# Kernel optimization log

Measured on AMD Instinct MI355X. Metric: run time of the kernel, lower is better.

Reference implementation:

```python
import jax, jax.numpy as jnp
import numpy as np

B, N, K = 4, 8192, 16
D_POINTS, D_MODEL, INIT_DIM = 64, 64, 3

def _lin(key, din, dout, bias=True):
    k1, k2 = jax.random.split(key)
    s = 1.0 / np.sqrt(din)
    w = jax.random.uniform(k1, (din, dout), minval=-s, maxval=s, dtype=jnp.float32)
    if not bias:
        return w
    b = jax.random.uniform(k2, (dout,), minval=-s, maxval=s, dtype=jnp.float32)
    return w, b

def setup_inputs() -> dict:
    key = jax.random.key(0)
    ks = jax.random.split(key, 12)
    xyz = jax.random.normal(ks[0], (B, N, INIT_DIM), dtype=jnp.float32)
    features = jax.random.normal(ks[1], (B, N, D_POINTS), dtype=jnp.float32)
    knn_idx = jax.random.randint(ks[2], (B, N, K), 0, N)
    fc1_w, fc1_b = _lin(ks[3], D_POINTS, D_MODEL)
    fc2_w, fc2_b = _lin(ks[4], D_MODEL, D_POINTS)
    d1_w, d1_b = _lin(ks[5], INIT_DIM, D_MODEL)
    d2_w, d2_b = _lin(ks[6], D_MODEL, D_MODEL)
    g1_w, g1_b = _lin(ks[7], D_MODEL, D_MODEL)
    g2_w, g2_b = _lin(ks[8], D_MODEL, D_MODEL)
    wq = _lin(ks[9], D_MODEL, D_MODEL, bias=False)
    wk = _lin(ks[10], D_MODEL, D_MODEL, bias=False)
    wv = _lin(ks[11], D_MODEL, D_MODEL, bias=False)
    return dict(xyz=xyz, features=features, knn_idx=knn_idx,
                fc1_w=fc1_w, fc1_b=fc1_b, fc2_w=fc2_w, fc2_b=fc2_b,
                d1_w=d1_w, d1_b=d1_b, d2_w=d2_w, d2_b=d2_b,
                g1_w=g1_w, g1_b=g1_b, g2_w=g2_w, g2_b=g2_b,
                wq=wq, wk=wk, wv=wv)

def _index_points(x, idx):
    # x: (B, N, D), idx: (B, M, K) -> (B, M, K, D)
    return jax.vmap(lambda xb, ib: xb[ib])(x, idx)

def reference(xyz, features, knn_idx,
              fc1_w, fc1_b, fc2_w, fc2_b,
              d1_w, d1_b, d2_w, d2_b,
              g1_w, g1_b, g2_w, g2_b,
              wq, wk, wv):
    idx = knn_idx[:, :, :K]
    knn_xyz = _index_points(xyz, idx)                      # (B,N,K,3)
    pre = features
    x = features @ fc1_w + fc1_b                           # (B,N,d_model)
    q = x @ wq                                             # (B,N,d_model)
    k = _index_points(x @ wk, idx)                         # (B,N,K,d_model)
    v = _index_points(x @ wv, idx)                         # (B,N,K,d_model)
    rel = xyz[:, :, None, :] - knn_xyz                     # (B,N,K,3)
    pos_enc = jax.nn.relu(rel @ d1_w + d1_b) @ d2_w + d2_b # (B,N,K,d_model)
    h = q[:, :, None, :] - k + pos_enc
    attn = jax.nn.relu(h @ g1_w + g1_b) @ g2_w + g2_b      # (B,N,K,d_model)
    attn = jax.nn.softmax(attn / np.sqrt(D_MODEL), axis=-2)
    res = jnp.einsum('bmnf,bmnf->bmf', attn, v + pos_enc)  # (B,N,d_model)
    res = res @ fc2_w + fc2_b + pre                        # (B,N,d_points)
    return res, attn
```

## Files before the change

### kernel.cpp

```cpp
#include <hip/hip_runtime.h>
#include <hip/hip_bf16.h>

#define B_    4
#define N_    8192
#define TOT   (B_*N_)
#define KNN_  16
#define PPW   8
#define PITCH 80

typedef _Float16 half8  __attribute__((ext_vector_type(8)));
typedef float    floatx4 __attribute__((ext_vector_type(4)));

#define MFMA16(A, Bv, C) __builtin_amdgcn_mfma_f32_16x16x32_f16((A), (Bv), (C), 0, 0, 0)

__device__ __forceinline__ void lds_fence(){
  asm volatile("s_waitcnt lgkmcnt(0)" ::: "memory");
}
__device__ __forceinline__ half8 h8_load_f32(const float* __restrict__ p){
  float4 a = *(const float4*)p;
  float4 b = *(const float4*)(p + 4);
  half8 r;
  r[0] = (_Float16)a.x; r[1] = (_Float16)a.y; r[2] = (_Float16)a.z; r[3] = (_Float16)a.w;
  r[4] = (_Float16)b.x; r[5] = (_Float16)b.y; r[6] = (_Float16)b.z; r[7] = (_Float16)b.w;
  return r;
}
__device__ __forceinline__ void store8f(float* __restrict__ p, half8 v){
  float4 a = {(float)v[0], (float)v[1], (float)v[2], (float)v[3]};
  float4 b = {(float)v[4], (float)v[5], (float)v[6], (float)v[7]};
  *(float4*)p = a;
  *(float4*)(p + 4) = b;
}

__device__ void fill_w64(half8* dst, const float* __restrict__ W, int tid){
  for (int i = tid; i < 512; i += 256){
    int lane = i & 63, nt = (i >> 6) & 3, kt = i >> 8;
    int n  = nt*16 + (lane & 15);
    int kb = kt*32 + ((lane >> 4) & 3)*8;
    half8 v;
    #pragma unroll
    for (int j = 0; j < 8; j++) v[j] = (_Float16)W[(kb + j)*64 + n];
    dst[i] = v;
  }
}
__device__ void fill_d1(half8* dst, const float* __restrict__ W, int tid){
  if (tid < 256){
    int lane = tid & 63, nt = tid >> 6;
    int n  = nt*16 + (lane & 15);
    int kb = ((lane >> 4) & 3)*8;
    half8 v;
    #pragma unroll
    for (int j = 0; j < 8; j++){
      int k = kb + j;
      v[j] = (k < 3) ? (_Float16)W[k*64 + n] : (_Float16)0.0f;
    }
    dst[tid] = v;
  }
}

__global__ __launch_bounds__(256, 2) void k1_qkv(
    const float* __restrict__ feat, const float* __restrict__ fc1w, const float* __restrict__ fc1b,
    const float* __restrict__ wqw, const float* __restrict__ wkw, const float* __restrict__ wvw,
    _Float16* __restrict__ qws, _Float16* __restrict__ kws, _Float16* __restrict__ vws)
{
  __shared__ half8 Sfc1[512], Sq[512], Sk[512], Sv[512];
  __shared__ alignas(16) _Float16 xt[4][16*PITCH];
  const int tid = threadIdx.x;
  fill_w64(Sfc1, fc1w, tid);
  fill_w64(Sq, wqw, tid);
  fill_w64(Sk, wkw, tid);
  fill_w64(Sv, wvw, tid);
  __syncthreads();

  const int wave = tid >> 6, lane = tid & 63, quad = lane >> 4, m16 = lane & 15;
  _Float16* tx = &xt[wave][0];
  const int rowbase = blockIdx.x*64 + wave*16;
  float fb[4];
  #pragma unroll
  for (int nt = 0; nt < 4; nt++) fb[nt] = fc1b[nt*16 + m16];

  const int arow = rowbase + m16;
  half8 Fa0 = h8_load_f32(&feat[arow*64 + quad*8]);
  half8 Fa1 = h8_load_f32(&feat[arow*64 + 32 + quad*8]);
  const floatx4 z4 = {0.f, 0.f, 0.f, 0.f};

  #pragma unroll
  for (int nt = 0; nt < 4; nt++){
    floatx4 acc = MFMA16(Fa0, Sfc1[nt*64 + lane], z4);
    acc = MFMA16(Fa1, Sfc1[(4 + nt)*64 + lane], acc);
    const int col = nt*16 + m16;
    #pragma unroll
    for (int r = 0; r < 4; r++)
      tx[(quad*4 + r)*PITCH + col] = (_Float16)(acc[r] + fb[nt]);
  }
  lds_fence();
  const half8 Ax0 = *(const half8*)&tx[m16*PITCH + quad*8];
  const half8 Ax1 = *(const half8*)&tx[m16*PITCH + 32 + quad*8];

#define EMIT_QKV(S, OUT)                                                      \
  { _Pragma("unroll")                                                         \
    for (int nt = 0; nt < 4; nt++){                                           \
      floatx4 acc = MFMA16(Ax0, S[nt*64 + lane], z4);                         \
      acc = MFMA16(Ax1, S[(4 + nt)*64 + lane], acc);                          \
      _Pragma("unroll")                                                       \
      for (int r = 0; r < 4; r++)                                             \
        OUT[(rowbase + quad*4 + r)*64 + nt*16 + m16] = (_Float16)acc[r];      \
    } }
  EMIT_QKV(Sq, qws)
  EMIT_QKV(Sk, kws)
  EMIT_QKV(Sv, vws)
#undef EMIT_QKV
}

__global__ __launch_bounds__(256, 2) void k2_point(
    const float* __restrict__ xyz, const int* __restrict__ knn,
    const float* __restrict__ d1w, const float* __restrict__ d1b,
    const float* __restrict__ d2w, const float* __restrict__ d2b,
    const float* __restrict__ g1w, const float* __restrict__ g1b,
    const float* __restrict__ g2w, const float* __restrict__ g2b,
    const _Float16* __restrict__ qws, const _Float16* __restrict__ kws,
    const _Float16* __restrict__ vws,
    _Float16* __restrict__ r0, float* __restrict__ attn_out)
{
  __shared__ half8 Sd1[256], Sd2[512], Sg1[512], Sg2[512];
  __shared__ alignas(16) _Float16 tiles[4][2][16*PITCH];
  const int tid = threadIdx.x;
  fill_d1(Sd1, d1w, tid);
  fill_w64(Sd2, d2w, tid);
  fill_w64(Sg1, g1w, tid);
  fill_w64(Sg2, g2w, tid);
  __syncthreads();

  const int wave = tid >> 6, lane = tid & 63, quad = lane >> 4, m16 = lane & 15;
  _Float16* tA = &tiles[wave][0][0];
  _Float16* tB = &tiles[wave][1][0];

  half8 Fd1[4], Fd2[2][4], Fg1[2][4], Fg2[2][4];
  #pragma unroll
  for (int nt = 0; nt < 4; nt++){
    Fd1[nt] = Sd1[nt*64 + lane];
    #pragma unroll
    for (int kt = 0; kt < 2; kt++){
      Fd2[kt][nt] = Sd2[(kt*4 + nt)*64 + lane];
      Fg1[kt][nt] = Sg1[(kt*4 + nt)*64 + lane];
      Fg2[kt][nt] = Sg2[(kt*4 + nt)*64 + lane];
    }
  }
  float bd1[4], bd2[4], bg1[4], bg2[4];
  #pragma unroll
  for (int nt = 0; nt < 4; nt++){
    const int c = nt*16 + m16;
    bd1[nt] = d1b[c]; bd2[nt] = d2b[c];
    bg1[nt] = g1b[c]; bg2[nt] = g2b[c];
  }
  const floatx4 z4 = {0.f, 0.f, 0.f, 0.f};

  for (int p = 0; p < PPW; p++){
    const int gpt  = blockIdx.x*(4*PPW) + wave*PPW + p;
    const int b    = gpt >> 13;
    const int idxm = knn[gpt*KNN_ + m16];
    const int grow = b*N_ + idxm;

    half8 Ar;
    #pragma unroll
    for (int j = 0; j < 8; j++) Ar[j] = (_Float16)0.0f;
    if (quad == 0){
      #pragma unroll
      for (int j = 0; j < 3; j++)
        Ar[j] = (_Float16)(xyz[gpt*3 + j] - xyz[grow*3 + j]);
    }

    #pragma unroll
    for (int nt = 0; nt < 4; nt++){
      floatx4 acc = MFMA16(Ar, Fd1[nt], z4);
      const int col = nt*16 + m16;
      #pragma unroll
      for (int r = 0; r < 4; r++){
        float t = acc[r] + bd1[nt];
        tA[(quad*4 + r)*PITCH + col] = (_Float16)(t > 0.f ? t : 0.f);
      }
    }
    lds_fence();
    const half8 At0 = *(const half8*)&tA[m16*PITCH + quad*8];
    const half8 At1 = *(const half8*)&tA[m16*PITCH + 32 + quad*8];

    #pragma unroll
    for (int nt = 0; nt < 4; nt++){
      floatx4 acc = MFMA16(At0, Fd2[0][nt], z4);
      acc = MFMA16(At1, Fd2[1][nt], acc);
      const int col = nt*16 + m16;
      #pragma unroll
      for (int r = 0; r < 4; r++)
        tB[(quad*4 + r)*PITCH + col] = (_Float16)(acc[r] + bd2[nt]);
    }
    lds_fence();
    const half8 Pa0 = *(const half8*)&tB[m16*PITCH + quad*8];
    const half8 Pa1 = *(const half8*)&tB[m16*PITCH + 32 + quad*8];

    const half8 Ka0 = *(const half8*)&kws[grow*64 + quad*8];
    const half8 Ka1 = *(const half8*)&kws[grow*64 + 32 + quad*8];
    const half8 Qa0 = *(const half8*)&qws[gpt*64 + quad*8];
    const half8 Qa1 = *(const half8*)&qws[gpt*64 + 32 + quad*8];
    const half8 H0 = Qa0 - Ka0 + Pa0;
    const half8 H1 = Qa1 - Ka1 + Pa1;

    #pragma unroll
    for (int nt = 0; nt < 4; nt++){
      floatx4 acc = MFMA16(H0, Fg1[0][nt], z4);
      acc = MFMA16(H1, Fg1[1][nt], acc);
      const int col = nt*16 + m16;
      #pragma unroll
      for (int r = 0; r < 4; r++){
        float t = acc[r] + bg1[nt];
        tA[(quad*4 + r)*PITCH + col] = (_Float16)(t > 0.f ? t : 0.f);
      }
    }
    lds_fence();
    const half8 U0 = *(const half8*)&tA[m16*PITCH + quad*8];
    const half8 U1 = *(const half8*)&tA[m16*PITCH + 32 + quad*8];

    float A2[4][4];
    #pragma unroll
    for (int nt = 0; nt < 4; nt++){
      floatx4 acc = MFMA16(U0, Fg2[0][nt], z4);
      acc = MFMA16(U1, Fg2[1][nt], acc);
      #pragma unroll
      for (int r = 0; r < 4; r++) A2[nt][r] = acc[r] + bg2[nt];
    }

    #pragma unroll
    for (int nt = 0; nt < 4; nt++){
      float mx = fmaxf(fmaxf(A2[nt][0], A2[nt][1]), fmaxf(A2[nt][2], A2[nt][3]));
      mx = fmaxf(mx, __shfl_xor(mx, 16));
      mx = fmaxf(mx, __shfl_xor(mx, 32));
      float s = 0.f;
      #pragma unroll
      for (int r = 0; r < 4; r++){
        float e = expf((A2[nt][r] - mx)*0.125f);
        A2[nt][r] = e; s += e;
      }
      s += __shfl_xor(s, 16);
      s += __shfl_xor(s, 32);
      const float inv = 1.0f / s;
      const int col = nt*16 + m16;
      #pragma unroll
      for (int r = 0; r < 4; r++)
        tA[(quad*4 + r)*PITCH + col] = (_Float16)(A2[nt][r]*inv);
    }
    lds_fence();
    const half8 Aa0 = *(const half8*)&tA[m16*PITCH + quad*8];
    const half8 Aa1 = *(const half8*)&tA[m16*PITCH + 32 + quad*8];
    const half8 Va0 = *(const half8*)&vws[grow*64 + quad*8];
    const half8 Va1 = *(const half8*)&vws[grow*64 + 32 + quad*8];

    float* ap = attn_out + ((size_t)gpt*KNN_ + m16)*64;
    store8f(ap + quad*8, Aa0);
    store8f(ap + 32 + quad*8, Aa1);

    float w0[8], w1[8];
    #pragma unroll
    for (int j = 0; j < 8; j++){
      w0[j] = (float)Aa0[j] * ((float)Va0[j] + (float)Pa0[j]);
      w1[j] = (float)Aa1[j] * ((float)Va1[j] + (float)Pa1[j]);
    }
    #pragma unroll
    for (int mask = 1; mask < 16; mask <<= 1){
      #pragma unroll
      for (int j = 0; j < 8; j++){
        w0[j] += __shfl_xor(w0[j], mask);
        w1[j] += __shfl_xor(w1[j], mask);
      }
    }
    if (m16 == 0){
      half8 o0, o1;
      #pragma unroll
      for (int j = 0; j < 8; j++){ o0[j] = (_Float16)w0[j]; o1[j] = (_Float16)w1[j]; }
      *(half8*)&r0[gpt*64 + quad*8] = o0;
      *(half8*)&r0[gpt*64 + 32 + quad*8] = o1;
    }
  }
}

__global__ __launch_bounds__(256, 2) void k3_fc2(
    const _Float16* __restrict__ r0, const float* __restrict__ fc2w,
    const float* __restrict__ fc2b, const float* __restrict__ feat,
    float* __restrict__ out_res)
{
  __shared__ half8 S[512];
  const int tid = threadIdx.x;
  fill_w64(S, fc2w, tid);
  __syncthreads();

  const int wave = tid >> 6, lane = tid & 63, quad = lane >> 4, m16 = lane & 15;
  const int rowbase = blockIdx.x*64 + wave*16;
  float fb[4];
  #pragma unroll
  for (int nt = 0; nt < 4; nt++) fb[nt] = fc2b[nt*16 + m16];

  const half8 A0 = *(const half8*)&r0[(rowbase + m16)*64 + quad*8];
  const half8 A1 = *(const half8*)&r0[(rowbase + m16)*64 + 32 + quad*8];
  const floatx4 z4 = {0.f, 0.f, 0.f, 0.f};

  #pragma unroll
  for (int nt = 0; nt < 4; nt++){
    floatx4 acc = MFMA16(A0, S[nt*64 + lane], z4);
    acc = MFMA16(A1, S[(4 + nt)*64 + lane], acc);
    #pragma unroll
    for (int r = 0; r < 4; r++){
      const int rowg = rowbase + quad*4 + r;
      const int col  = nt*16 + m16;
      out_res[rowg*64 + col] = acc[r] + fb[nt] + feat[rowg*64 + col];
    }
  }
}

extern "C" void kernel_launch(void* const* d_in, const int* in_sizes, int n_in,
                              void* d_out, int out_size, void* d_ws, size_t ws_size,
                              hipStream_t stream)
{
  (void)in_sizes; (void)n_in; (void)out_size; (void)ws_size;
  const float* xyz  = (const float*)d_in[0];
  const float* feat = (const float*)d_in[1];
  const int*   knn  = (const int*)d_in[2];
  const float* fc1w = (const float*)d_in[3];
  const float* fc1b = (const float*)d_in[4];
  const float* fc2w = (const float*)d_in[5];
  const float* fc2b = (const float*)d_in[6];
  const float* d1w  = (const float*)d_in[7];
  const float* d1b  = (const float*)d_in[8];
  const float* d2w  = (const float*)d_in[9];
  const float* d2b  = (const float*)d_in[10];
  const float* g1w  = (const float*)d_in[11];
  const float* g1b  = (const float*)d_in[12];
  const float* g2w  = (const float*)d_in[13];
  const float* g2b  = (const float*)d_in[14];
  const float* wq   = (const float*)d_in[15];
  const float* wk   = (const float*)d_in[16];
  const float* wv   = (const float*)d_in[17];

  _Float16* ws  = (_Float16*)d_ws;
  _Float16* qws = ws;
  _Float16* kws = ws + (size_t)TOT*64;
  _Float16* vws = ws + (size_t)2*TOT*64;
  _Float16* r0  = ws + (size_t)3*TOT*64;

  float* out      = (float*)d_out;
  float* out_res  = out;
  float* out_attn = out + (size_t)TOT*64;

  k1_qkv<<<TOT/64, 256, 0, stream>>>(feat, fc1w, fc1b, wq, wk, wv, qws, kws, vws);
  k2_point<<<TOT/(4*PPW), 256, 0, stream>>>(xyz, knn, d1w, d1b, d2w, d2b,
                                            g1w, g1b, g2w, g2b,
                                            qws, kws, vws, r0, out_attn);
  k3_fc2<<<TOT/64, 256, 0, stream>>>(r0, fc2w, fc2b, feat, out_res);
}
```

Measured before the change: 268.5 us.

## Load weights directly into registers, shrink LDS tiles, prefetch gathers, use fp16 reduction

k2 and k3 now load their MFMA weight fragments straight from global memory into registers, dropping the LDS weight staging and block barrier. k2 reuses a single tile per wave with a smaller pitch and raises the occupancy hint. It also preloads the kNN indices and issues the K/V/Q gathers at the start of each point iteration to hide latency. The softmax uses exp2 with a folded scale, and the weighted sum over neighbours is reduced with packed half2 shuffles instead of fp32. The fp16 accumulation lowers precision, and register pressure may rise.

```diff
diff --git a/kernel.cpp b/kernel.cpp
--- a/kernel.cpp
+++ b/kernel.cpp
@@ -6,9 +6,11 @@
 #define TOT   (B_*N_)
 #define KNN_  16
 #define PPW   8
-#define PITCH 80
+#define PITCH 68
 
 typedef _Float16 half8  __attribute__((ext_vector_type(8)));
+typedef _Float16 half4  __attribute__((ext_vector_type(4)));
+typedef _Float16 half2v __attribute__((ext_vector_type(2)));
 typedef float    floatx4 __attribute__((ext_vector_type(4)));
 
 #define MFMA16(A, Bv, C) __builtin_amdgcn_mfma_f32_16x16x32_f16((A), (Bv), (C), 0, 0, 0)
@@ -30,6 +32,35 @@
   *(float4*)p = a;
   *(float4*)(p + 4) = b;
 }
+__device__ __forceinline__ half8 tile_read8(const _Float16* t, int idx){
+  half4 lo = *(const half4*)(t + idx);
+  half4 hi = *(const half4*)(t + idx + 4);
+  half8 r;
+  #pragma unroll
+  for (int j = 0; j < 4; j++){ r[j] = lo[j]; r[4+j] = hi[j]; }
+  return r;
+}
+__device__ __forceinline__ half8 wfrag(const float* __restrict__ W, int kb, int n){
+  half8 v;
+  #pragma unroll
+  for (int j = 0; j < 8; j++) v[j] = (_Float16)W[(kb + j)*64 + n];
+  return v;
+}
+__device__ __forceinline__ half8 red_over_m16(half8 x){
+  union { half8 h; int i[4]; } u; u.h = x;
+  #pragma unroll
+  for (int mask = 1; mask < 16; mask <<= 1){
+    #pragma unroll
+    for (int t = 0; t < 4; t++){
+      int o = __shfl_xor(u.i[t], mask);
+      union { int i; half2v h; } a, b;
+      a.i = u.i[t]; b.i = o;
+      a.h = a.h + b.h;
+      u.i[t] = a.i;
+    }
+  }
+  return u.h;
+}
 
 __device__ void fill_w64(half8* dst, const float* __restrict__ W, int tid){
   for (int i = tid; i < 512; i += 256){
@@ -40,20 +71,6 @@
     #pragma unroll
     for (int j = 0; j < 8; j++) v[j] = (_Float16)W[(kb + j)*64 + n];
     dst[i] = v;
-  }
-}
-__device__ void fill_d1(half8* dst, const float* __restrict__ W, int tid){
-  if (tid < 256){
-    int lane = tid & 63, nt = tid >> 6;
-    int n  = nt*16 + (lane & 15);
-    int kb = ((lane >> 4) & 3)*8;
-    half8 v;
-    #pragma unroll
-    for (int j = 0; j < 8; j++){
-      int k = kb + j;
-      v[j] = (k < 3) ? (_Float16)W[k*64 + n] : (_Float16)0.0f;
-    }
-    dst[tid] = v;
   }
 }
 
@@ -93,8 +110,8 @@
       tx[(quad*4 + r)*PITCH + col] = (_Float16)(acc[r] + fb[nt]);
   }
   lds_fence();
-  const half8 Ax0 = *(const half8*)&tx[m16*PITCH + quad*8];
-  const half8 Ax1 = *(const half8*)&tx[m16*PITCH + 32 + quad*8];
+  const half8 Ax0 = tile_read8(tx, m16*PITCH + quad*8);
+  const half8 Ax1 = tile_read8(tx, m16*PITCH + 32 + quad*8);
 
 #define EMIT_QKV(S, OUT)                                                      \
   { _Pragma("unroll")                                                         \
@@ -111,7 +128,7 @@
 #undef EMIT_QKV
 }
 
-__global__ __launch_bounds__(256, 2) void k2_point(
+__global__ __launch_bounds__(256, 3) void k2_point(
     const float* __restrict__ xyz, const int* __restrict__ knn,
     const float* __restrict__ d1w, const float* __restrict__ d1b,
     const float* __restrict__ d2w, const float* __restrict__ d2b,
@@ -121,28 +138,30 @@
     const _Float16* __restrict__ vws,
     _Float16* __restrict__ r0, float* __restrict__ attn_out)
 {
-  __shared__ half8 Sd1[256], Sd2[512], Sg1[512], Sg2[512];
-  __shared__ alignas(16) _Float16 tiles[4][2][16*PITCH];
+  __shared__ alignas(16) _Float16 tiles[4][16*PITCH];
   const int tid = threadIdx.x;
-  fill_d1(Sd1, d1w, tid);
-  fill_w64(Sd2, d2w, tid);
-  fill_w64(Sg1, g1w, tid);
-  fill_w64(Sg2, g2w, tid);
-  __syncthreads();
-
   const int wave = tid >> 6, lane = tid & 63, quad = lane >> 4, m16 = lane & 15;
-  _Float16* tA = &tiles[wave][0][0];
-  _Float16* tB = &tiles[wave][1][0];
+  _Float16* tA = &tiles[wave][0];
 
   half8 Fd1[4], Fd2[2][4], Fg1[2][4], Fg2[2][4];
   #pragma unroll
   for (int nt = 0; nt < 4; nt++){
-    Fd1[nt] = Sd1[nt*64 + lane];
+    const int n = nt*16 + m16;
+    {
+      half8 v;
+      #pragma unroll
+      for (int j = 0; j < 8; j++){
+        int k = quad*8 + j;
+        v[j] = (k < 3) ? (_Float16)d1w[k*64 + n] : (_Float16)0.0f;
+      }
+      Fd1[nt] = v;
+    }
     #pragma unroll
     for (int kt = 0; kt < 2; kt++){
-      Fd2[kt][nt] = Sd2[(kt*4 + nt)*64 + lane];
-      Fg1[kt][nt] = Sg1[(kt*4 + nt)*64 + lane];
-      Fg2[kt][nt] = Sg2[(kt*4 + nt)*64 + lane];
+      const int kb = kt*32 + quad*8;
+      Fd2[kt][nt] = wfrag(d2w, kb, n);
+      Fg1[kt][nt] = wfrag(g1w, kb, n);
+      Fg2[kt][nt] = wfrag(g2w, kb, n);
     }
   }
   float bd1[4], bd2[4], bg1[4], bg2[4];
@@ -153,20 +172,36 @@
     bg1[nt] = g1b[c]; bg2[nt] = g2b[c];
   }
   const floatx4 z4 = {0.f, 0.f, 0.f, 0.f};
-
+  const float SC = 0.18033688f;
+
+  const int base = blockIdx.x*(4*PPW) + wave*PPW;
+  const int bb   = (base >> 13) << 13;
+
+  int idxs[PPW];
+  #pragma unroll
+  for (int p = 0; p < PPW; p++) idxs[p] = knn[(base + p)*KNN_ + m16];
+
+  #pragma unroll
   for (int p = 0; p < PPW; p++){
-    const int gpt  = blockIdx.x*(4*PPW) + wave*PPW + p;
-    const int b    = gpt >> 13;
-    const int idxm = knn[gpt*KNN_ + m16];
-    const int grow = b*N_ + idxm;
+    const int gpt  = base + p;
+    const int grow = bb + idxs[p];
+
+    const half8 Ka0 = *(const half8*)&kws[grow*64 + quad*8];
+    const half8 Ka1 = *(const half8*)&kws[grow*64 + 32 + quad*8];
+    const half8 Va0 = *(const half8*)&vws[grow*64 + quad*8];
+    const half8 Va1 = *(const half8*)&vws[grow*64 + 32 + quad*8];
+    const half8 Qa0 = *(const half8*)&qws[gpt*64 + quad*8];
+    const half8 Qa1 = *(const half8*)&qws[gpt*64 + 32 + quad*8];
+    float rel[3];
+    #pragma unroll
+    for (int j = 0; j < 3; j++) rel[j] = xyz[gpt*3 + j] - xyz[grow*3 + j];
 
     half8 Ar;
     #pragma unroll
     for (int j = 0; j < 8; j++) Ar[j] = (_Float16)0.0f;
     if (quad == 0){
       #pragma unroll
-      for (int j = 0; j < 3; j++)
-        Ar[j] = (_Float16)(xyz[gpt*3 + j] - xyz[grow*3 + j]);
+      for (int j = 0; j < 3; j++) Ar[j] = (_Float16)rel[j];
     }
 
     #pragma unroll
@@ -180,8 +215,8 @@
       }
     }
     lds_fence();
-    const half8 At0 = *(const half8*)&tA[m16*PITCH + quad*8];
-    const half8 At1 = *(const half8*)&tA[m16*PITCH + 32 + quad*8];
+    const half8 At0 = tile_read8(tA, m16*PITCH + quad*8);
+    const half8 At1 = tile_read8(tA, m16*PITCH + 32 + quad*8);
 
     #pragma unroll
     for (int nt = 0; nt < 4; nt++){
@@ -190,16 +225,12 @@
       const int col = nt*16 + m16;
       #pragma unroll
       for (int r = 0; r < 4; r++)
-        tB[(quad*4 + r)*PITCH + col] = (_Float16)(acc[r] + bd2[nt]);
+        tA[(quad*4 + r)*PITCH + col] = (_Float16)(acc[r] + bd2[nt]);
     }
     lds_fence();
-    const half8 Pa0 = *(const half8*)&tB[m16*PITCH + quad*8];
-    const half8 Pa1 = *(const half8*)&tB[m16*PITCH + 32 + quad*8];
-
-    const half8 Ka0 = *(const half8*)&kws[grow*64 + quad*8];
-    const half8 Ka1 = *(const half8*)&kws[grow*64 + 32 + quad*8];
-    const half8 Qa0 = *(const half8*)&qws[gpt*64 + quad*8];
-    const half8 Qa1 = *(const half8*)&qws[gpt*64 + 32 + quad*8];
+    const half8 Pa0 = tile_read8(tA, m16*PITCH + quad*8);
+    const half8 Pa1 = tile_read8(tA, m16*PITCH + 32 + quad*8);
+
     const half8 H0 = Qa0 - Ka0 + Pa0;
     const half8 H1 = Qa1 - Ka1 + Pa1;
 
@@ -215,8 +246,8 @@
       }
     }
     lds_fence();
-    const half8 U0 = *(const half8*)&tA[m16*PITCH + quad*8];
-    const half8 U1 = *(const half8*)&tA[m16*PITCH + 32 + quad*8];
+    const half8 U0 = tile_read8(tA, m16*PITCH + quad*8);
+    const half8 U1 = tile_read8(tA, m16*PITCH + 32 + quad*8);
 
     float A2[4][4];
     #pragma unroll
@@ -235,7 +266,7 @@
       float s = 0.f;
       #pragma unroll
       for (int r = 0; r < 4; r++){
-        float e = expf((A2[nt][r] - mx)*0.125f);
+        float e = exp2f((A2[nt][r] - mx)*SC);
         A2[nt][r] = e; s += e;
       }
       s += __shfl_xor(s, 16);
@@ -247,51 +278,40 @@
         tA[(quad*4 + r)*PITCH + col] = (_Float16)(A2[nt][r]*inv);
     }
     lds_fence();
-    const half8 Aa0 = *(const half8*)&tA[m16*PITCH + quad*8];
-    const half8 Aa1 = *(const half8*)&tA[m16*PITCH + 32 + quad*8];
-    const half8 Va0 = *(const half8*)&vws[grow*64 + quad*8];
-    const half8 Va1 = *(const half8*)&vws[grow*64 + 32 + quad*8];
+    const half8 Aa0 = tile_read8(tA, m16*PITCH + quad*8);
+    const half8 Aa1 = tile_read8(tA, m16*PITCH + 32 + quad*8);
 
     float* ap = attn_out + ((size_t)gpt*KNN_ + m16)*64;
     store8f(ap + quad*8, Aa0);
     store8f(ap + 32 + quad*8, Aa1);
 
-    float w0[8], w1[8];
-    #pragma unroll
-    for (int j = 0; j < 8; j++){
-      w0[j] = (float)Aa0[j] * ((float)Va0[j] + (float)Pa0[j]);
-      w1[j] = (float)Aa1[j] * ((float)Va1[j] + (float)Pa1[j]);
-    }
-    #pragma unroll
-    for (int mask = 1; mask < 16; mask <<= 1){
-      #pragma unroll
-      for (int j = 0; j < 8; j++){
-        w0[j] += __shfl_xor(w0[j], mask);
-        w1[j] += __shfl_xor(w1[j], mask);
-      }
-    }
+    const half8 W0 = Aa0 * (Va0 + Pa0);
+    const half8 W1 = Aa1 * (Va1 + Pa1);
+    const half8 R0 = red_over_m16(W0);
+    const half8 R1 = red_over_m16(W1);
     if (m16 == 0){
-      half8 o0, o1;
-      #pragma unroll
-      for (int j = 0; j < 8; j++){ o0[j] = (_Float16)w0[j]; o1[j] = (_Float16)w1[j]; }
-      *(half8*)&r0[gpt*64 + quad*8] = o0;
-      *(half8*)&r0[gpt*64 + 32 + quad*8] = o1;
-    }
-  }
-}
-
-__global__ __launch_bounds__(256, 2) void k3_fc2(
+      *(half8*)&r0[gpt*64 + quad*8] = R0;
+      *(half8*)&r0[gpt*64 + 32 + quad*8] = R1;
+    }
+  }
+}
+
+__global__ __launch_bounds__(256, 4) void k3_fc2(
     const _Float16* __restrict__ r0, const float* __restrict__ fc2w,
     const float* __restrict__ fc2b, const float* __restrict__ feat,
     float* __restrict__ out_res)
 {
-  __shared__ half8 S[512];
   const int tid = threadIdx.x;
-  fill_w64(S, fc2w, tid);
-  __syncthreads();
-
   const int wave = tid >> 6, lane = tid & 63, quad = lane >> 4, m16 = lane & 15;
   const int rowbase = blockIdx.x*64 + wave*16;
+
+  half8 S[2][4];
+  #pragma unroll
+  for (int kt = 0; kt < 2; kt++)
+    #pragma unroll
+    for (int nt = 0; nt < 4; nt++)
+      S[kt][nt] = wfrag(fc2w, kt*32 + quad*8, nt*16 + m16);
+
   float fb[4];
   #pragma unroll
   for (int nt = 0; nt < 4; nt++) fb[nt] = fc2b[nt*16 + m16];
@@ -302,8 +322,8 @@
 
   #pragma unroll
   for (int nt = 0; nt < 4; nt++){
-    floatx4 acc = MFMA16(A0, S[nt*64 + lane], z4);
-    acc = MFMA16(A1, S[(4 + nt)*64 + lane], acc);
+    floatx4 acc = MFMA16(A0, S[0][nt], z4);
+    acc = MFMA16(A1, S[1][nt], acc);
     #pragma unroll
     for (int r = 0; r < 4; r++){
       const int rowg = rowbase + quad*4 + r;
```

Result: slower. 391.5 us (+45.8%).
